# Optimization experiments

Measured on AMD Instinct MI355X. Metric: run time of the kernel, lower is better.

The kernel has to match this reference:

```python
import jax, jax.numpy as jnp
import numpy as np

HID = 512      # hidden_dim
MID = 256      # hid_dim
COND_D = 256   # condition_op_dim
OP_D = 32      # operator_len
EX_D = 32      # extra_info_num
L, N, T = 16, 1024, 8
EPS = 1e-5


def _lstm_cell(x_proj, h, c, Whh, bhh):
    # x_proj: precomputed x @ Wih.T + bih, shape [B, 4H]
    gates = x_proj + h @ Whh.T + bhh
    i, f, g, o = jnp.split(gates, 4, axis=-1)
    i = jax.nn.sigmoid(i); f = jax.nn.sigmoid(f)
    g = jnp.tanh(g); o = jax.nn.sigmoid(o)
    c = f * c + i * g
    h = o * jnp.tanh(c)
    return h, c


def _batchnorm(x, gamma, beta):
    mu = x.mean(0)
    var = x.var(0)  # biased, matches PyTorch training-mode normalization
    return gamma * (x - mu) * jax.lax.rsqrt(var + EPS) + beta


def setup_inputs() -> dict:
    key = jax.random.key(0)
    ks = jax.random.split(key, 24)
    s = lambda *sh: 0.05
    inp = {
        'operators': jax.random.normal(ks[0], (L, N, OP_D), jnp.float32),
        'extra_infos': jax.random.normal(ks[1], (L, N, EX_D), jnp.float32),
        'conditions': jax.random.normal(ks[2], (L, N, T, COND_D), jnp.float32),
        'condition_masks': jnp.ones((L, N, 1), jnp.float32),
        'mapping': jax.random.randint(ks[3], (L, N, 2), 0, N + 1, jnp.int32).astype(jnp.int64),
        'lstm1_Wih': jax.random.normal(ks[4], (4 * HID, COND_D), jnp.float32) * 0.05,
        'lstm1_Whh': jax.random.normal(ks[5], (4 * HID, HID), jnp.float32) * 0.05,
        'lstm1_bih': jnp.zeros((4 * HID,), jnp.float32),
        'lstm1_bhh': jnp.zeros((4 * HID,), jnp.float32),
        'cond_W': jax.random.normal(ks[6], (MID, HID), jnp.float32) * 0.05,
        'cond_b': jnp.zeros((MID,), jnp.float32),
        'bn1_g': jnp.ones((MID,), jnp.float32),
        'bn1_b': jnp.zeros((MID,), jnp.float32),
        'lstm2_Wih': jax.random.normal(ks[7], (4 * HID, OP_D + EX_D + MID), jnp.float32) * 0.05,
        'lstm2_Whh': jax.random.normal(ks[8], (4 * HID, HID), jnp.float32) * 0.05,
        'lstm2_bih': jnp.zeros((4 * HID,), jnp.float32),
        'lstm2_bhh': jnp.zeros((4 * HID,), jnp.float32),
        'bn2_g': jnp.ones((HID,), jnp.float32),
        'bn2_b': jnp.zeros((HID,), jnp.float32),
    }
    return inp


def reference(operators, extra_infos, conditions, condition_masks, mapping,
              lstm1_Wih, lstm1_Whh, lstm1_bih, lstm1_bhh,
              cond_W, cond_b, bn1_g, bn1_b,
              lstm2_Wih, lstm2_Whh, lstm2_bih, lstm2_bhh,
              bn2_g, bn2_b):
    B = L * N
    x = conditions.reshape(B, T, COND_D)
    # lstm1 over conditions; precompute input projections for all steps
    xp = jnp.einsum('btd,gd->btg', x, lstm1_Wih) + lstm1_bih  # [B,T,4H]

    def step1(carry, xt):
        h, c = carry
        h, c = _lstm_cell(xt, h, c, lstm1_Whh, lstm1_bhh)
        return (h, c), None

    h0 = jnp.zeros((B, HID), xp.dtype)
    (h1, _), _ = jax.lax.scan(step1, (h0, h0), jnp.swapaxes(xp, 0, 1))

    last = jax.nn.relu(h1 @ cond_W.T + cond_b)       # [B, MID]
    last = _batchnorm(last, bn1_g, bn1_b).reshape(L, N, MID)

    out = jnp.concatenate([operators, extra_infos, last], axis=2)  # [L,N,IN2]
    xp2 = jnp.einsum('lnd,gd->lng', out, lstm2_Wih) + lstm2_bih    # [L,N,4H]

    hz = jnp.zeros((N, HID), xp2.dtype)
    h, c = _lstm_cell(xp2[L - 1], hz, hz, lstm2_Whh, lstm2_bhh)

    mapping = mapping.astype(jnp.int32)
    levels = jnp.arange(L - 2, -1, -1)

    def tree_step(carry, idx):
        h, c = carry
        mp = mapping[idx]  # [N,2]
        pad = jnp.zeros((1, HID), h.dtype)
        ph = jnp.concatenate([pad, h], 0)  # [N+1,H]
        pc = jnp.concatenate([pad, c], 0)
        h = (ph[mp[:, 0]] + ph[mp[:, 1]]) * 0.5
        c = (pc[mp[:, 0]] + pc[mp[:, 1]]) * 0.5
        h, c = _lstm_cell(xp2[idx], h, c, lstm2_Whh, lstm2_bhh)
        return (h, c), None

    (h, c), _ = jax.lax.scan(tree_step, (h, c), levels)

    # batch_size == N since all operator rows are nonzero
    return _batchnorm(h, bn2_g, bn2_b)  # [N, HID]
```

## Files before the change

kernel.cpp:

```cpp
#include <hip/hip_runtime.h>
#include <hip/hip_bf16.h>
#include <stdint.h>


typedef __bf16 bf16;
typedef __bf16 bf16x8 __attribute__((ext_vector_type(8)));
typedef float f32x4 __attribute__((ext_vector_type(4)));

#define HIDDEN 512

__device__ __forceinline__ float fast_sig(float x) { return 1.f / (1.f + __expf(-x)); }
__device__ __forceinline__ float fast_tanh(float x) {
  float e = __expf(2.f * x);
  return 1.f - 2.f / (e + 1.f);
}

__device__ __forceinline__ void async16(const bf16* g, bf16* l) {
  __builtin_amdgcn_global_load_lds(
      (const __attribute__((address_space(1))) void*)g,
      (__attribute__((address_space(3))) void*)l, 16, 0, 0);
}

__device__ __forceinline__ void cvt_one(const float* __restrict__ src,
                                        bf16* __restrict__ dst, size_t i) {
  float4 a = *(const float4*)(src + i);
  float4 b = *(const float4*)(src + i + 4);
  bf16x8 r;
  r[0] = (bf16)a.x; r[1] = (bf16)a.y; r[2] = (bf16)a.z; r[3] = (bf16)a.w;
  r[4] = (bf16)b.x; r[5] = (bf16)b.y; r[6] = (bf16)b.z; r[7] = (bf16)b.w;
  *(bf16x8*)(dst + i) = r;
}

__global__ void prep(const float* conds, bf16* conds_b,
                     const float* s0, bf16* d0, const float* s1, bf16* d1,
                     const float* s2, bf16* d2, const float* s3, bf16* d3,
                     const float* s4, bf16* d4, const float* s5, bf16* d5,
                     const float* s6, bf16* d6,
                     const int* map, int* flags) {
  int b = blockIdx.x;
  int tid = threadIdx.x;
  if (b < 2176) {
    int g = b * 256 + tid;
    const float* s; bf16* d; int off;
    if      (g < 65536)  { s = s0; d = d0; off = g; }
    else if (g < 131072) { s = s1; d = d1; off = g - 65536; }
    else if (g < 196608) { s = s2; d = d2; off = g - 131072; }
    else if (g < 327680) { s = s3; d = d3; off = g - 196608; }
    else if (g < 344064) { s = s4; d = d4; off = g - 327680; }
    else if (g < 425984) { s = s5; d = d5; off = g - 344064; }
    else if (g < 557056) { s = s6; d = d6; off = g - 425984; }
    else return;
    cvt_one(s, d, (size_t)off * 8);
  } else if (b == 2176) {
    __shared__ int any;
    if (tid == 0) any = 0;
    __syncthreads();
    int loc = 0;
    for (int i = tid; i < 16384; i += 256) loc |= map[2 * i + 1];
    if (loc) atomicOr(&any, 1);
    __syncthreads();
    if (tid == 0) flags[0] = (any == 0) ? 1 : 0;
  } else {
    size_t i = ((size_t)(b - 2177) * 256 + tid) * 8;
    cvt_one(conds, conds_b, i);
  }
}

template <int MT, int KT0, int KT1>
__global__ __launch_bounds__(256, 2) void cell_gemm(
    const bf16* __restrict__ A0, int a0off, int a0s,
    const bf16* __restrict__ A1, int a1s,
    const bf16* __restrict__ B0, int b0s,
    const bf16* __restrict__ B1, int b1s,
    const float* __restrict__ bias0, const float* __restrict__ bias1,
    const float* __restrict__ c_prev,
    float* __restrict__ c_out,
    bf16* __restrict__ h_b16)
{
  constexpr int BM = MT * 32;
  __shared__ __align__(16) bf16 sA[BM * 64];
  __shared__ __align__(16) bf16 sB[128 * 64];
  const int tid = threadIdx.x;
  const int lane = tid & 63;
  const int quad = lane >> 4, cl = lane & 15;
  const int wave = tid >> 6;
  const int wr = wave >> 1, wc = wave & 1;
  const int bm0 = blockIdx.x * BM;
  const int j0 = blockIdx.y * 32;

  const bf16* ra[MT][2];
  const bf16* rb[4][2];
#pragma unroll
  for (int mi = 0; mi < MT; ++mi)
#pragma unroll
    for (int kh = 0; kh < 2; ++kh) {
      int row = wr * (MT * 16) + mi * 16 + cl;
      ra[mi][kh] = &sA[row * 64 + (((kh * 4 + quad) ^ (row & 7))) * 8];
    }
#pragma unroll
  for (int g = 0; g < 4; ++g)
#pragma unroll
    for (int kh = 0; kh < 2; ++kh) {
      int row = g * 32 + wc * 16 + cl;
      rb[g][kh] = &sB[row * 64 + (((kh * 4 + quad) ^ (row & 7))) * 8];
    }

  f32x4 acc[MT][4];
#pragma unroll
  for (int mi = 0; mi < MT; ++mi)
#pragma unroll
    for (int g = 0; g < 4; ++g) acc[mi][g] = f32x4{0.f, 0.f, 0.f, 0.f};

  const bf16* pa[MT];
  const bf16* pb[4];
#pragma unroll
  for (int ia = 0; ia < MT; ++ia) {
    int e = ia * 256 + tid, row = e >> 3, sl = e & 7;
    pa[ia] = A0 + (size_t)((bm0 + row) * a0s + a0off + (sl ^ (row & 7)) * 8);
  }
#pragma unroll
  for (int ib = 0; ib < 4; ++ib) {
    int e = ib * 256 + tid, row = e >> 3, sl = e & 7;
    int wrow = (row >> 5) * HIDDEN + j0 + (row & 31);
    pb[ib] = B0 + (size_t)(wrow * b0s + (sl ^ (row & 7)) * 8);
  }

  auto ktile = [&]() {
#pragma unroll
    for (int ia = 0; ia < MT; ++ia) {
      async16(pa[ia], sA + (ia * 256 + tid) * 8);
      pa[ia] += 64;
    }
#pragma unroll
    for (int ib = 0; ib < 4; ++ib) {
      async16(pb[ib], sB + (ib * 256 + tid) * 8);
      pb[ib] += 64;
    }
    __syncthreads();
#pragma unroll
    for (int kh = 0; kh < 2; ++kh) {
      bf16x8 af[MT], bfr[4];
#pragma unroll
      for (int mi = 0; mi < MT; ++mi) af[mi] = *(const bf16x8*)ra[mi][kh];
#pragma unroll
      for (int g = 0; g < 4; ++g) bfr[g] = *(const bf16x8*)rb[g][kh];
#pragma unroll
      for (int mi = 0; mi < MT; ++mi)
#pragma unroll
        for (int g = 0; g < 4; ++g)
          acc[mi][g] = __builtin_amdgcn_mfma_f32_16x16x32_bf16(af[mi], bfr[g], acc[mi][g], 0, 0, 0);
    }
    __syncthreads();
  };

  for (int kt = 0; kt < KT0; ++kt) ktile();
  if (KT1 > 0) {
#pragma unroll
    for (int ia = 0; ia < MT; ++ia) {
      int e = ia * 256 + tid, row = e >> 3, sl = e & 7;
      pa[ia] = A1 + (size_t)((bm0 + row) * a1s + (sl ^ (row & 7)) * 8);
    }
#pragma unroll
    for (int ib = 0; ib < 4; ++ib) {
      int e = ib * 256 + tid, row = e >> 3, sl = e & 7;
      int wrow = (row >> 5) * HIDDEN + j0 + (row & 31);
      pb[ib] = B1 + (size_t)(wrow * b1s + (sl ^ (row & 7)) * 8);
    }
    for (int kt = 0; kt < KT1; ++kt) ktile();
  }

  const int j = j0 + wc * 16 + cl;
  float bI = bias0[j] + bias1[j];
  float bF = bias0[HIDDEN + j] + bias1[HIDDEN + j];
  float bG = bias0[2 * HIDDEN + j] + bias1[2 * HIDDEN + j];
  float bO = bias0[3 * HIDDEN + j] + bias1[3 * HIDDEN + j];
#pragma unroll
  for (int mi = 0; mi < MT; ++mi) {
    int rb_ = bm0 + wr * (MT * 16) + mi * 16 + quad * 4;
#pragma unroll
    for (int r = 0; r < 4; ++r) {
      int row = rb_ + r;
      float iv = fast_sig(acc[mi][0][r] + bI);
      float fv = fast_sig(acc[mi][1][r] + bF);
      float gv = fast_tanh(acc[mi][2][r] + bG);
      float ov = fast_sig(acc[mi][3][r] + bO);
      float cp = c_prev ? c_prev[(size_t)row * HIDDEN + j] : 0.f;
      float cn = fv * cp + iv * gv;
      float hn = ov * fast_tanh(cn);
      c_out[(size_t)row * HIDDEN + j] = cn;
      h_b16[(size_t)row * HIDDEN + j] = (bf16)hn;
    }
  }
}

__global__ __launch_bounds__(256, 2) void cell_tree_f(
    const int* __restrict__ map, const int* __restrict__ flags, int level,
    const bf16* __restrict__ h_src, const float* __restrict__ c_src,
    const bf16* __restrict__ W,
    const float* __restrict__ bhh,
    const bf16* __restrict__ xp,
    float* __restrict__ c_out,
    bf16* __restrict__ h_out,
    float* __restrict__ h_f32)
{
  __shared__ __align__(16) bf16 sA[32 * 512];
  __shared__ __align__(16) bf16 sB[128 * 64];
  const int tid = threadIdx.x;
  const int lane = tid & 63;
  const int quad = lane >> 4, cl = lane & 15;
  const int wave = tid >> 6;
  const int wr = wave >> 1, wc = wave & 1;
  const int bm0 = blockIdx.x * 32;
  const int j0 = blockIdx.y * 32;
  const int fl = flags[0];

  {
    int grow = tid >> 3;
    int w = tid & 7;
    int n = bm0 + grow;
    long mbase = (long)level * 2048 + n * 2;
    int m0, m1;
    if (fl) { m0 = map[mbase * 2]; m1 = map[mbase * 2 + 2]; }
    else    { m0 = map[mbase];     m1 = map[mbase + 1]; }
    const bf16* s0 = h_src + (size_t)(m0 ? m0 - 1 : 0) * HIDDEN;
    const bf16* s1 = h_src + (size_t)(m1 ? m1 - 1 : 0) * HIDDEN;
    float f0 = m0 ? 0.5f : 0.f;
    float f1 = m1 ? 0.5f : 0.f;
    int sw = grow & 7;
    bf16* drow = sA + grow * 512;
#pragma unroll
    for (int g = 0; g < 8; ++g) {
      int slot = g * 8 + w;
      bf16x8 a = *(const bf16x8*)(s0 + slot * 8);
      bf16x8 b = *(const bf16x8*)(s1 + slot * 8);
      bf16x8 r;
#pragma unroll
      for (int e = 0; e < 8; ++e)
        r[e] = (bf16)(f0 * (float)a[e] + f1 * (float)b[e]);
      *(bf16x8*)(drow + (g * 8 + (w ^ sw)) * 8) = r;
    }
  }

  const bf16* ra[2];
#pragma unroll
  for (int kh = 0; kh < 2; ++kh) {
    int row = wr * 16 + cl;
    ra[kh] = &sA[row * 512 + (((kh * 4 + quad) ^ (row & 7))) * 8];
  }
  const bf16* rb[4][2];
#pragma unroll
  for (int g = 0; g < 4; ++g)
#pragma unroll
    for (int kh = 0; kh < 2; ++kh) {
      int row = g * 32 + wc * 16 + cl;
      rb[g][kh] = &sB[row * 64 + (((kh * 4 + quad) ^ (row & 7))) * 8];
    }

  f32x4 acc[4];
#pragma unroll
  for (int g = 0; g < 4; ++g) acc[g] = f32x4{0.f, 0.f, 0.f, 0.f};

  const bf16* pb[4];
#pragma unroll
  for (int ib = 0; ib < 4; ++ib) {
    int e = ib * 256 + tid, row = e >> 3, sl = e & 7;
    int wrow = (row >> 5) * HIDDEN + j0 + (row & 31);
    pb[ib] = W + (size_t)(wrow * HIDDEN + (sl ^ (row & 7)) * 8);
  }

  for (int kt = 0; kt < 8; ++kt) {
#pragma unroll
    for (int ib = 0; ib < 4; ++ib) {
      async16(pb[ib], sB + (ib * 256 + tid) * 8);
      pb[ib] += 64;
    }
    __syncthreads();
#pragma unroll
    for (int kh = 0; kh < 2; ++kh) {
      bf16x8 af = *(const bf16x8*)(ra[kh] + kt * 64);
#pragma unroll
      for (int g = 0; g < 4; ++g) {
        bf16x8 bfr = *(const bf16x8*)rb[g][kh];
        acc[g] = __builtin_amdgcn_mfma_f32_16x16x32_bf16(af, bfr, acc[g], 0, 0, 0);
      }
    }
    __syncthreads();
  }

  const int j = j0 + wc * 16 + cl;
  float bI = bhh[j], bF = bhh[HIDDEN + j];
  float bG = bhh[2 * HIDDEN + j], bO = bhh[3 * HIDDEN + j];
  int rb0 = bm0 + wr * 16 + quad * 4;
#pragma unroll
  for (int r = 0; r < 4; ++r) {
    int row = rb0 + r;
    long mbase = (long)level * 2048 + row * 2;
    int m0, m1;
    if (fl) { m0 = map[mbase * 2]; m1 = map[mbase * 2 + 2]; }
    else    { m0 = map[mbase];     m1 = map[mbase + 1]; }
    float c0 = m0 ? c_src[(size_t)(m0 - 1) * HIDDEN + j] : 0.f;
    float c1 = m1 ? c_src[(size_t)(m1 - 1) * HIDDEN + j] : 0.f;
    float cp = 0.5f * (c0 + c1);
    const bf16* xr = xp + (size_t)row * 2048;
    float gi = acc[0][r] + bI + (float)xr[j];
    float gf = acc[1][r] + bF + (float)xr[HIDDEN + j];
    float gg = acc[2][r] + bG + (float)xr[2 * HIDDEN + j];
    float go = acc[3][r] + bO + (float)xr[3 * HIDDEN + j];
    float cn = fast_sig(gf) * cp + fast_sig(gi) * fast_tanh(gg);
    float hn = fast_sig(go) * fast_tanh(cn);
    c_out[(size_t)row * HIDDEN + j] = cn;
    h_out[(size_t)row * HIDDEN + j] = (bf16)hn;
    if (h_f32) h_f32[(size_t)row * HIDDEN + j] = hn;
  }
}

template <int MT>
__global__ __launch_bounds__(256, 2) void plain_gemm(
    const bf16* __restrict__ A0, int a0s, int a0kt,
    const bf16* __restrict__ A1, int a1s, int a1kt,
    const bf16* __restrict__ A2, int a2s, int a2kt,
    const bf16* __restrict__ B, int bs,
    const float* __restrict__ bias, int do_relu,
    bf16* __restrict__ outh, int Ntot)
{
  constexpr int BM = MT * 32;
  __shared__ __align__(16) bf16 sA[BM * 32];
  __shared__ __align__(16) bf16 sB[128 * 32];
  const int tid = threadIdx.x;
  const int lane = tid & 63;
  const int quad = lane >> 4, cl = lane & 15;
  const int wave = tid >> 6;
  const int wr = wave >> 1, wc = wave & 1;
  const int bm0 = blockIdx.x * BM;
  const int bn0 = blockIdx.y * 128;

  f32x4 acc[MT][4];
#pragma unroll
  for (int mi = 0; mi < MT; ++mi)
#pragma unroll
    for (int ni = 0; ni < 4; ++ni) acc[mi][ni] = f32x4{0.f, 0.f, 0.f, 0.f};

  const int nkt = a0kt + a1kt + a2kt;
  for (int kt = 0; kt < nkt; ++kt) {
    const bf16* abase; int astr, acol;
    if (kt < a0kt)            { abase = A0; astr = a0s; acol = kt * 32; }
    else if (kt < a0kt + a1kt){ abase = A1; astr = a1s; acol = (kt - a0kt) * 32; }
    else                      { abase = A2; astr = a2s; acol = (kt - a0kt - a1kt) * 32; }
#pragma unroll
    for (int ia = 0; ia < MT / 2; ++ia) {
      int e = ia * 256 + tid;
      int row = e >> 2, sl = e & 3;
      int src = sl ^ ((row >> 1) & 3);
      async16(abase + (size_t)(bm0 + row) * astr + acol + src * 8, sA + e * 8);
    }
#pragma unroll
    for (int ib = 0; ib < 2; ++ib) {
      int e = ib * 256 + tid;
      int row = e >> 2, sl = e & 3;
      int src = sl ^ ((row >> 1) & 3);
      async16(B + (size_t)(bn0 + row) * bs + kt * 32 + src * 8, sB + e * 8);
    }
    __syncthreads();
    bf16x8 af[MT], bfr[4];
#pragma unroll
    for (int mi = 0; mi < MT; ++mi) {
      int row = wr * (MT * 16) + mi * 16 + cl;
      int sl = quad ^ ((row >> 1) & 3);
      af[mi] = *(const bf16x8*)&sA[row * 32 + sl * 8];
    }
#pragma unroll
    for (int ni = 0; ni < 4; ++ni) {
      int row = wc * 64 + ni * 16 + cl;
      int sl = quad ^ ((row >> 1) & 3);
      bfr[ni] = *(const bf16x8*)&sB[row * 32 + sl * 8];
    }
#pragma unroll
    for (int mi = 0; mi < MT; ++mi)
#pragma unroll
      for (int ni = 0; ni < 4; ++ni)
        acc[mi][ni] = __builtin_amdgcn_mfma_f32_16x16x32_bf16(af[mi], bfr[ni], acc[mi][ni], 0, 0, 0);
    __syncthreads();
  }

#pragma unroll
  for (int mi = 0; mi < MT; ++mi) {
    int rb = bm0 + wr * (MT * 16) + mi * 16 + quad * 4;
#pragma unroll
    for (int ni = 0; ni < 4; ++ni) {
      int col = bn0 + wc * 64 + ni * 16 + cl;
      float bv = bias ? bias[col] : 0.f;
#pragma unroll
      for (int r = 0; r < 4; ++r) {
        int row = rb + r;
        float v = acc[mi][ni][r] + bv;
        if (do_relu) v = fmaxf(v, 0.f);
        outh[(size_t)row * Ntot + col] = (bf16)v;
      }
    }
  }
}

__global__ void cell0(const bf16* __restrict__ xp,
                      const float* __restrict__ bhh,
                      bf16* __restrict__ h, float* __restrict__ c)
{
  int n = blockIdx.x, j = threadIdx.x;
  float g[4];
#pragma unroll
  for (int k = 0; k < 4; ++k)
    g[k] = (float)xp[(size_t)n * 2048 + k * 512 + j] + bhh[k * 512 + j];
  float cv = fast_sig(g[0]) * fast_tanh(g[2]);
  h[(size_t)n * HIDDEN + j] = (bf16)(fast_sig(g[3]) * fast_tanh(cv));
  c[(size_t)n * HIDDEN + j] = cv;
}

__global__ void bn_reduce_b16(const bf16* __restrict__ x, int rpb, int F,
                              float* __restrict__ partials) {
  int col = threadIdx.x, b = blockIdx.x;
  const bf16* p = x + (size_t)b * rpb * F + col;
  float s = 0.f, q = 0.f;
  for (int r = 0; r < rpb; ++r) { float v = (float)p[(size_t)r * F]; s += v; q += v * v; }
  partials[(size_t)b * 2 * F + col] = s;
  partials[(size_t)b * 2 * F + F + col] = q;
}

__global__ void bn_reduce_f32(const float* __restrict__ x, int rpb, int F,
                              float* __restrict__ partials) {
  int col = threadIdx.x, b = blockIdx.x;
  const float* p = x + (size_t)b * rpb * F + col;
  float s = 0.f, q = 0.f;
  for (int r = 0; r < rpb; ++r) { float v = p[(size_t)r * F]; s += v; q += v * v; }
  partials[(size_t)b * 2 * F + col] = s;
  partials[(size_t)b * 2 * F + F + col] = q;
}

__global__ void bn_final(const float* __restrict__ partials, int nb, int F,
                         const float* __restrict__ g, const float* __restrict__ b,
                         float invB, float* __restrict__ scale, float* __restrict__ shift) {
  int j = threadIdx.x;
  float s = 0.f, q = 0.f;
  for (int i = 0; i < nb; ++i) {
    s += partials[(size_t)i * 2 * F + j];
    q += partials[(size_t)i * 2 * F + F + j];
  }
  float mu = s * invB;
  float var = fmaxf(q * invB - mu * mu, 0.f);
  float sc = g[j] * rsqrtf(var + 1e-5f);
  scale[j] = sc;
  shift[j] = b[j] - sc * mu;
}

__global__ void bn_apply_mid(const bf16* __restrict__ x, const float* __restrict__ scale,
                             const float* __restrict__ shift, int Fmask, size_t total,
                             bf16* __restrict__ out) {
  for (size_t i = blockIdx.x * (size_t)blockDim.x + threadIdx.x; i < total;
       i += (size_t)gridDim.x * blockDim.x) {
    int j = (int)(i & (size_t)Fmask);
    out[i] = (bf16)(scale[j] * (float)x[i] + shift[j]);
  }
}

__global__ void bn_apply_out(const float* __restrict__ x, const float* __restrict__ scale,
                             const float* __restrict__ shift, int Fmask, size_t total,
                             float* __restrict__ out) {
  for (size_t i = blockIdx.x * (size_t)blockDim.x + threadIdx.x; i < total;
       i += (size_t)gridDim.x * blockDim.x) {
    int j = (int)(i & (size_t)Fmask);
    out[i] = scale[j] * x[i] + shift[j];
  }
}

extern "C" void kernel_launch(void* const* d_in, const int* in_sizes, int n_in,
                              void* d_out, int out_size, void* d_ws, size_t ws_size,
                              hipStream_t stream) {
  const float* operators = (const float*)d_in[0];
  const float* extras    = (const float*)d_in[1];
  const float* conds     = (const float*)d_in[2];
  const int*   mapping   = (const int*)d_in[4];
  const float* b1ih = (const float*)d_in[7];
  const float* b1hh = (const float*)d_in[8];
  const float* condb = (const float*)d_in[10];
  const float* bn1g = (const float*)d_in[11];
  const float* bn1b = (const float*)d_in[12];
  const float* b2ih = (const float*)d_in[15];
  const float* b2hh = (const float*)d_in[16];
  const float* bn2g = (const float*)d_in[17];
  const float* bn2b = (const float*)d_in[18];

  char* ws = (char*)d_ws;
  size_t o = 0;
  auto alloc = [&](size_t bytes) {
    char* p = ws + o;
    o += (bytes + 255) & ~(size_t)255;
    return p;
  };
  bf16* conds_b = (bf16*)alloc((size_t)33554432 * 2);
  bf16* ops_b   = (bf16*)alloc((size_t)524288 * 2);
  bf16* ext_b   = (bf16*)alloc((size_t)524288 * 2);
  bf16* w1ih_b  = (bf16*)alloc((size_t)524288 * 2);
  bf16* w1hh_b  = (bf16*)alloc((size_t)1048576 * 2);
  bf16* condw_b = (bf16*)alloc((size_t)131072 * 2);
  bf16* w2ih_b  = (bf16*)alloc((size_t)655360 * 2);
  bf16* w2hh_b  = (bf16*)alloc((size_t)1048576 * 2);
  bf16* h1[2];
  h1[0] = (bf16*)alloc((size_t)16384 * 512 * 2);
  h1[1] = (bf16*)alloc((size_t)16384 * 512 * 2);
  float* c1 = (float*)alloc((size_t)16384 * 512 * 4);
  bf16* last_relu = (bf16*)alloc((size_t)16384 * 256 * 2);
  bf16* last_bn = (bf16*)alloc((size_t)16384 * 256 * 2);
  bf16* hbuf0 = (bf16*)alloc((size_t)1024 * 512 * 2);
  bf16* hbuf1 = (bf16*)alloc((size_t)1024 * 512 * 2);
  float* cbuf0 = (float*)alloc((size_t)1024 * 512 * 4);
  float* cbuf1 = (float*)alloc((size_t)1024 * 512 * 4);
  float* h2f = (float*)alloc((size_t)1024 * 512 * 4);
  float* partials = (float*)alloc((size_t)64 * 1024 * 4);
  float* scale1 = (float*)alloc(256 * 4);
  float* shift1 = (float*)alloc(256 * 4);
  float* scale2 = (float*)alloc(512 * 4);
  float* shift2 = (float*)alloc(512 * 4);
  int* flags = (int*)alloc(256);
  bf16* xp2 = (bf16*)alloc((size_t)16384 * 2048 * 2);

  prep<<<18561, 256, 0, stream>>>(
      conds, conds_b,
      operators, ops_b, extras, ext_b,
      (const float*)d_in[5], w1ih_b, (const float*)d_in[6], w1hh_b,
      (const float*)d_in[9], condw_b, (const float*)d_in[13], w2ih_b,
      (const float*)d_in[14], w2hh_b,
      mapping, flags);

  cell_gemm<4, 4, 0><<<dim3(128, 16), 256, 0, stream>>>(
      conds_b, 0, 2048, nullptr, 512,
      w1ih_b, 256, w1hh_b, 512,
      b1ih, b1hh, nullptr, c1, h1[1]);
  for (int t = 1; t < 8; ++t) {
    cell_gemm<4, 4, 8><<<dim3(128, 16), 256, 0, stream>>>(
        conds_b, t * 256, 2048, h1[t & 1], 512,
        w1ih_b, 256, w1hh_b, 512,
        b1ih, b1hh, c1, c1, h1[(t + 1) & 1]);
  }

  plain_gemm<2><<<dim3(256, 2), 256, 0, stream>>>(
      h1[0], 512, 16, nullptr, 0, 0, nullptr, 0, 0,
      condw_b, 512, condb, 1, last_relu, 256);
  bn_reduce_b16<<<64, 256, 0, stream>>>(last_relu, 256, 256, partials);
  bn_final<<<1, 256, 0, stream>>>(partials, 64, 256, bn1g, bn1b, 1.f / 16384.f, scale1, shift1);
  bn_apply_mid<<<1024, 256, 0, stream>>>(last_relu, scale1, shift1, 255,
                                         (size_t)16384 * 256, last_bn);

  plain_gemm<4><<<dim3(128, 16), 256, 0, stream>>>(
      ops_b, 32, 1, ext_b, 32, 1, last_bn, 256, 8,
      w2ih_b, 320, b2ih, 0, xp2, 2048);

  size_t lvl_sz = (size_t)1024 * 2048;
  bf16* hb[2] = {hbuf0, hbuf1};
  float* cb[2] = {cbuf0, cbuf1};
  cell0<<<1024, 512, 0, stream>>>(xp2 + 15 * lvl_sz, b2hh, hb[0], cb[0]);
  int cur = 0;
  for (int idx = 14; idx >= 0; --idx) {
    int nxt = cur ^ 1;
    cell_tree_f<<<dim3(32, 16), 256, 0, stream>>>(
        mapping, flags, idx, hb[cur], cb[cur], w2hh_b, b2hh,
        xp2 + (size_t)idx * lvl_sz, cb[nxt], hb[nxt],
        (idx == 0) ? h2f : nullptr);
    cur = nxt;
  }

  bn_reduce_f32<<<16, 512, 0, stream>>>(h2f, 64, 512, partials);
  bn_final<<<1, 512, 0, stream>>>(partials, 16, 512, bn2g, bn2b, 1.f / 1024.f, scale2, shift2);
  bn_apply_out<<<512, 256, 0, stream>>>(h2f, scale2, shift2, 511,
                                        (size_t)1024 * 512, (float*)d_out);
}
```

Measured before the change: 1.159 ms.

## Double-buffer LDS tiles in cell_gemm to overlap global loads with MFMA

Doubles the shared-memory A and B tiles and restructures the K loop into a prefetch pipeline. The next K tile is staged into the alternate buffer with async global-to-LDS loads while the current tile feeds the MFMAs. The switch from the A0/B0 to the A1/B1 operands now happens inside the unified loop. This aims to hide global load latency and removes one barrier per tile, at the cost of twice the LDS per block, which may limit occupancy.

```diff
diff --git a/kernel.cpp b/kernel.cpp
--- a/kernel.cpp
+++ b/kernel.cpp
@@ -78,8 +78,10 @@
     bf16* __restrict__ h_b16)
 {
   constexpr int BM = MT * 32;
-  __shared__ __align__(16) bf16 sA[BM * 64];
-  __shared__ __align__(16) bf16 sB[128 * 64];
+  constexpr int ABUF = BM * 64;
+  constexpr int BBUF = 128 * 64;
+  __shared__ __align__(16) bf16 sA[2 * ABUF];
+  __shared__ __align__(16) bf16 sB[2 * BBUF];
   const int tid = threadIdx.x;
   const int lane = tid & 63;
   const int quad = lane >> 4, cl = lane & 15;
@@ -88,21 +90,21 @@
   const int bm0 = blockIdx.x * BM;
   const int j0 = blockIdx.y * 32;
 
-  const bf16* ra[MT][2];
-  const bf16* rb[4][2];
+  int ra[MT][2];
+  int rb[4][2];
 #pragma unroll
   for (int mi = 0; mi < MT; ++mi)
 #pragma unroll
     for (int kh = 0; kh < 2; ++kh) {
       int row = wr * (MT * 16) + mi * 16 + cl;
-      ra[mi][kh] = &sA[row * 64 + (((kh * 4 + quad) ^ (row & 7))) * 8];
+      ra[mi][kh] = row * 64 + (((kh * 4 + quad) ^ (row & 7))) * 8;
     }
 #pragma unroll
   for (int g = 0; g < 4; ++g)
 #pragma unroll
     for (int kh = 0; kh < 2; ++kh) {
       int row = g * 32 + wc * 16 + cl;
-      rb[g][kh] = &sB[row * 64 + (((kh * 4 + quad) ^ (row & 7))) * 8];
+      rb[g][kh] = row * 64 + (((kh * 4 + quad) ^ (row & 7))) * 8;
     }
 
   f32x4 acc[MT][4];
@@ -125,48 +127,55 @@
     pb[ib] = B0 + (size_t)(wrow * b0s + (sl ^ (row & 7)) * 8);
   }
 
-  auto ktile = [&]() {
+  auto stage = [&](int buf) {
+    bf16* da = sA + buf * ABUF;
+    bf16* db = sB + buf * BBUF;
 #pragma unroll
     for (int ia = 0; ia < MT; ++ia) {
-      async16(pa[ia], sA + (ia * 256 + tid) * 8);
+      async16(pa[ia], da + (ia * 256 + tid) * 8);
       pa[ia] += 64;
     }
 #pragma unroll
     for (int ib = 0; ib < 4; ++ib) {
-      async16(pb[ib], sB + (ib * 256 + tid) * 8);
+      async16(pb[ib], db + (ib * 256 + tid) * 8);
       pb[ib] += 64;
     }
-    __syncthreads();
+  };
+
+  stage(0);
+
+  const int nt = KT0 + KT1;
+  for (int t = 0; t < nt; ++t) {
+    if (KT1 > 0 && t + 1 == KT0) {
+#pragma unroll
+      for (int ia = 0; ia < MT; ++ia) {
+        int e = ia * 256 + tid, row = e >> 3, sl = e & 7;
+        pa[ia] = A1 + (size_t)((bm0 + row) * a1s + (sl ^ (row & 7)) * 8);
+      }
+#pragma unroll
+      for (int ib = 0; ib < 4; ++ib) {
+        int e = ib * 256 + tid, row = e >> 3, sl = e & 7;
+        int wrow = (row >> 5) * HIDDEN + j0 + (row & 31);
+        pb[ib] = B1 + (size_t)(wrow * b1s + (sl ^ (row & 7)) * 8);
+      }
+    }
+    __syncthreads();
+    if (t + 1 < nt) stage((t + 1) & 1);
+    const bf16* baseA = sA + (t & 1) * ABUF;
+    const bf16* baseB = sB + (t & 1) * BBUF;
 #pragma unroll
     for (int kh = 0; kh < 2; ++kh) {
       bf16x8 af[MT], bfr[4];
 #pragma unroll
-      for (int mi = 0; mi < MT; ++mi) af[mi] = *(const bf16x8*)ra[mi][kh];
-#pragma unroll
-      for (int g = 0; g < 4; ++g) bfr[g] = *(const bf16x8*)rb[g][kh];
+      for (int mi = 0; mi < MT; ++mi) af[mi] = *(const bf16x8*)(baseA + ra[mi][kh]);
+#pragma unroll
+      for (int g = 0; g < 4; ++g) bfr[g] = *(const bf16x8*)(baseB + rb[g][kh]);
 #pragma unroll
       for (int mi = 0; mi < MT; ++mi)
 #pragma unroll
         for (int g = 0; g < 4; ++g)
           acc[mi][g] = __builtin_amdgcn_mfma_f32_16x16x32_bf16(af[mi], bfr[g], acc[mi][g], 0, 0, 0);
     }
-    __syncthreads();
-  };
-
-  for (int kt = 0; kt < KT0; ++kt) ktile();
-  if (KT1 > 0) {
-#pragma unroll
-    for (int ia = 0; ia < MT; ++ia) {
-      int e = ia * 256 + tid, row = e >> 3, sl = e & 7;
-      pa[ia] = A1 + (size_t)((bm0 + row) * a1s + (sl ^ (row & 7)) * 8);
-    }
-#pragma unroll
-    for (int ib = 0; ib < 4; ++ib) {
-      int e = ib * 256 + tid, row = e >> 3, sl = e & 7;
-      int wrow = (row >> 5) * HIDDEN + j0 + (row & 31);
-      pb[ib] = B1 + (size_t)(wrow * b1s + (sl ^ (row & 7)) * 8);
-    }
-    for (int kt = 0; kt < KT1; ++kt) ktile();
   }
 
   const int j = j0 + wc * 16 + cl;
```

After: 1.215 ms. 1.05x slower.
